# Performance work log

Measured on AMD Instinct MI355X. Metric: run time of the kernel, lower is better.

## Reference

```python
import jax, jax.numpy as jnp
import numpy as np

NUM_HEADS = 8

def _qkv(t, W, b, H):
    # t: [B, L, C] -> q, k, v each [B, H, L, D]
    B, L, C = t.shape
    D = C // H
    qkv = (t @ W + b).reshape(B, L, 3, H, D)
    qkv = jnp.moveaxis(qkv, 2, 0)           # [3, B, L, H, D]
    qkv = jnp.swapaxes(qkv, 2, 3)           # [3, B, H, L, D]
    return qkv[0], qkv[1], qkv[2]

def _attend(q, k, v, scale):
    # q,k,v: [B, H, L, D] -> [B, L, C]
    B, H, L, D = q.shape
    scores = jnp.einsum('bhqd,bhkd->bhqk', q, k) * scale
    attn = jax.nn.softmax(scores, axis=-1)
    out = jnp.einsum('bhqk,bhkd->bhqd', attn, v)
    return jnp.swapaxes(out, 1, 2).reshape(B, L, H * D)

def setup_inputs() -> dict:
    key = jax.random.key(0)
    ks = jax.random.split(key, 7)
    B, N, C = 8, 2048, 512
    s_in = 1.0 / np.sqrt(C)
    return {
        'x': jax.random.normal(ks[0], (B, N, C), dtype=jnp.float32),
        'W_rgb_qkv': jax.random.normal(ks[1], (C, 3 * C), dtype=jnp.float32) * s_in,
        'b_rgb_qkv': jax.random.normal(ks[2], (3 * C,), dtype=jnp.float32) * 0.02,
        'W_depth_qkv': jax.random.normal(ks[3], (C, 3 * C), dtype=jnp.float32) * s_in,
        'b_depth_qkv': jax.random.normal(ks[4], (3 * C,), dtype=jnp.float32) * 0.02,
        'W_proj': jax.random.normal(ks[5], (C, C), dtype=jnp.float32) * s_in,
        'b_proj': jax.random.normal(ks[6], (C,), dtype=jnp.float32) * 0.02,
    }

def reference(x, W_rgb_qkv, b_rgb_qkv, W_depth_qkv, b_depth_qkv, W_proj, b_proj):
    B, N, C = x.shape
    H = NUM_HEADS
    D = C // H
    scale = D ** -0.5
    L = N // 2
    rgb, depth = x[:, :L], x[:, L:]
    rq, rk, rv = _qkv(rgb, W_rgb_qkv, b_rgb_qkv, H)
    dq, dk, dv = _qkv(depth, W_depth_qkv, b_depth_qkv, H)
    # rgb queries attend to depth K/V (named depth_v in torch code)
    depth_out = _attend(rq, dk, dv, scale)
    # depth queries attend to rgb K/V (named rgb_v in torch code)
    rgb_out = _attend(dq, rk, rv, scale)
    out = jnp.concatenate([rgb_out, depth_out], axis=1)  # [B, N, C]
    return out @ W_proj + b_proj
```

## Files before the change

### kernel.cpp

```cpp
#include <hip/hip_runtime.h>
#include <hip/hip_bf16.h>

typedef __attribute__((ext_vector_type(8))) short s16x8;
typedef __attribute__((ext_vector_type(4))) float f32x4;

__device__ __forceinline__ ushort f2bf(float f) {
  union { float f; unsigned int u; } c; c.f = f;
  unsigned int u = c.u + 0x7fffu + ((c.u >> 16) & 1u);
  return (ushort)(u >> 16);
}

__device__ __forceinline__ unsigned int pack2(float lo, float hi) {
  __hip_bfloat162 b2 = __float22bfloat162_rn(make_float2(lo, hi));
  union { __hip_bfloat162 b; unsigned int u; } c; c.b = b2;
  return c.u;
}

__device__ __forceinline__ s16x8 ld16(const ushort* p) {
  union { uint4 u; s16x8 s; } c;
  c.u = *reinterpret_cast<const uint4*>(p);
  return c.s;
}

__device__ __forceinline__ f32x4 mfma16(s16x8 a, s16x8 b, f32x4 c) {
  return __builtin_amdgcn_mfma_f32_16x16x32_bf16(a, b, c, 0, 0, 0);
}

__device__ __forceinline__ float exp2fast(float x) { return __builtin_amdgcn_exp2f(x); }

__device__ __forceinline__ void gld_lds16(const void* g, void* l) {
  __builtin_amdgcn_global_load_lds(
      (const __attribute__((address_space(1))) void*)g,
      (__attribute__((address_space(3))) void*)l, 16, 0, 0);
}


__global__ __launch_bounds__(256) void k_prep(
    const float* __restrict__ x, ushort* __restrict__ xb,
    const float* __restrict__ Wr, ushort* __restrict__ WtR,
    const float* __restrict__ Wd, ushort* __restrict__ WtD,
    const float* __restrict__ Wp, ushort* __restrict__ WtP) {
  __shared__ float tile[32][33];
  int b = blockIdx.x, t = threadIdx.x;
  if (b < 8192) {
    int i = (b * 256 + t) * 4;
    float4 v = *reinterpret_cast<const float4*>(x + i);
    ushort4 o;
    o.x = f2bf(v.x); o.y = f2bf(v.y); o.z = f2bf(v.z); o.w = f2bf(v.w);
    *reinterpret_cast<ushort4*>(xb + i) = o;
    return;
  }
  b -= 8192;
  const float* src; ushort* dst; int N;
  if (b < 768)      { src = Wr; dst = WtR; N = 1536; }
  else if (b < 1536){ b -= 768;  src = Wd; dst = WtD; N = 1536; }
  else              { b -= 1536; src = Wp; dst = WtP; N = 512; }
  int nb = N >> 5;
  int n0 = (b % nb) * 32, k0 = (b / nb) * 32;
  int tx = t & 31, ty = t >> 5;
#pragma unroll
  for (int i = 0; i < 32; i += 8)
    tile[ty + i][tx] = src[(k0 + ty + i) * N + (n0 + tx)];
  __syncthreads();
#pragma unroll
  for (int i = 0; i < 32; i += 8)
    dst[(size_t)(n0 + ty + i) * 512 + (k0 + tx)] = f2bf(tile[tx][ty + i]);
}


__device__ __forceinline__ s16x8 lds_frag(const char* lds, int row, int c) {
  union { uint4 u; s16x8 s; } cv;
  cv.u = *reinterpret_cast<const uint4*>(lds + row * 128 + ((c ^ (row & 7)) * 16));
  return cv.s;
}

__device__ __forceinline__ s16x8 lds_frag32(const char* lds, int row, int c) {
  union { uint4 u; s16x8 s; } cv;
  cv.u = *reinterpret_cast<const uint4*>(lds + row * 64 + ((c ^ ((row >> 1) & 3)) * 16));
  return cv.s;
}

__device__ __forceinline__ void stage_lds(const ushort* __restrict__ src, int ld,
                                          char* ldsbase, int t) {
#pragma unroll
  for (int p = 0; p < 4; ++p) {
    int chunk = p * 256 + t;
    int r = chunk >> 3, cc = chunk & 7;
    gld_lds16(src + r * ld + ((cc ^ (r & 7)) * 8), ldsbase + (chunk & ~63) * 16);
  }
}


template <bool TRANS>
__global__ __launch_bounds__(256) void k_qkv(
    const ushort* __restrict__ xb, const ushort* __restrict__ WtR,
    const ushort* __restrict__ WtD, const float* __restrict__ bR,
    const float* __restrict__ bD, ushort* __restrict__ Qb,
    ushort* __restrict__ Kb, ushort* __restrict__ Vt) {
  __shared__ __align__(16) char lds[49152];
  int m0 = blockIdx.x * 128;
  int n0 = (TRANS ? 1024 : 0) + blockIdx.y * 128;
  int s = m0 >> 13, bb = (m0 >> 10) & 7, lbase = m0 & 1023;
  const ushort* A = xb + (size_t)(bb * 2048 + s * 1024 + lbase) * 512;
  const ushort* Wt = (s ? WtD : WtR) + (size_t)n0 * 512;
  const float* bias = s ? bD : bR;
  int t = threadIdx.x;
  int wid = t >> 6, ln = t & 15, g = (t & 63) >> 4;
  int wr = wid >> 1, wc = wid & 1;

  int r0 = t >> 2, c0 = t & 3;
  int r1 = (t + 256) >> 2, c1 = t & 3;
  int so0 = r0 * 512 + ((c0 ^ ((r0 >> 1) & 3)) * 8);
  int so1 = r1 * 512 + ((c1 ^ ((r1 >> 1) & 3)) * 8);
  int ldu = (t & ~63) * 16;

  const ushort* As = A;
  const ushort* Bs = Wt;
  char* b0 = lds;
  char* b1 = lds + 16384;
  char* b2 = lds + 32768;

  f32x4 acc[4][4] = {};

  gld_lds16(As + so0, b0 + ldu);
  gld_lds16(As + so1, b0 + 4096 + ldu);
  gld_lds16(Bs + so0, b0 + 8192 + ldu);
  gld_lds16(Bs + so1, b0 + 12288 + ldu);
  As += 32; Bs += 32;
  gld_lds16(As + so0, b1 + ldu);
  gld_lds16(As + so1, b1 + 4096 + ldu);
  gld_lds16(Bs + so0, b1 + 8192 + ldu);
  gld_lds16(Bs + so1, b1 + 12288 + ldu);
  As += 32; Bs += 32;
  asm volatile("s_waitcnt vmcnt(4)" ::: "memory");
  __builtin_amdgcn_sched_barrier(0);
  __builtin_amdgcn_s_barrier();
  __builtin_amdgcn_sched_barrier(0);

  for (int ks = 0; ks < 16; ++ks) {
    if (ks < 14) {
      gld_lds16(As + so0, b2 + ldu);
      gld_lds16(As + so1, b2 + 4096 + ldu);
      gld_lds16(Bs + so0, b2 + 8192 + ldu);
      gld_lds16(Bs + so1, b2 + 12288 + ldu);
      As += 32; Bs += 32;
    }
    s16x8 af[4], bf[4];
    __builtin_amdgcn_s_setprio(1);
#pragma unroll
    for (int mi = 0; mi < 4; ++mi) af[mi] = lds_frag32(b0, wr * 64 + mi * 16 + ln, g);
#pragma unroll
    for (int ni = 0; ni < 4; ++ni) bf[ni] = lds_frag32(b0 + 8192, wc * 64 + ni * 16 + ln, g);
#pragma unroll
    for (int mi = 0; mi < 4; ++mi)
#pragma unroll
      for (int ni = 0; ni < 4; ++ni)
        acc[mi][ni] = TRANS ? mfma16(bf[ni], af[mi], acc[mi][ni])
                            : mfma16(af[mi], bf[ni], acc[mi][ni]);
    __builtin_amdgcn_s_setprio(0);

    if (ks < 15) {
      if (ks < 14) {
        asm volatile("s_waitcnt vmcnt(4)" ::: "memory");
      } else {
        asm volatile("s_waitcnt vmcnt(0)" ::: "memory");
      }
      __builtin_amdgcn_sched_barrier(0);
      __builtin_amdgcn_s_barrier();
      __builtin_amdgcn_sched_barrier(0);
    }
    char* tmp = b0; b0 = b1; b1 = b2; b2 = tmp;
  }

  int hb_base = (s * 8 + bb) * 8;
  if (!TRANS) {
    bool isK = (n0 >> 9) != 0;
    ushort* dst = isK ? Kb : Qb;
    float sc = isK ? 1.0f : 0.18033688011112042f;
#pragma unroll
    for (int mi = 0; mi < 4; ++mi)
#pragma unroll
      for (int ni = 0; ni < 4; ++ni) {
        f32x4 v = acc[mi][ni];
        int col = n0 + wc * 64 + ni * 16 + ln;
        int h = (col >> 6) & 7, d = col & 63;
        float bv = bias[col];
        ushort* hp = dst + ((size_t)(hb_base + h) << 16);
        int lr = lbase + wr * 64 + mi * 16 + g * 4;
#pragma unroll
        for (int j = 0; j < 4; ++j) hp[(lr + j) * 64 + d] = f2bf((v[j] + bv) * sc);
      }
  } else {
    __syncthreads();
    ushort* et = (ushort*)lds;
#pragma unroll
    for (int mi = 0; mi < 4; ++mi) {
      int ll = wr * 64 + mi * 16 + ln;
      int lpl = (ll & ~63) | (ll & 0x23) | ((ll & 0x0C) << 1) | ((ll & 0x10) >> 2);
      int chunk = lpl >> 3, within = lpl & 7;
#pragma unroll
      for (int ni = 0; ni < 4; ++ni) {
        f32x4 v = acc[mi][ni];
        int crb = wc * 64 + ni * 16 + g * 4;
#pragma unroll
        for (int j = 0; j < 4; ++j) {
          int cr = crb + j;
          float bv = bias[n0 + cr];
          *(ushort*)((char*)et + cr * 256 + ((chunk ^ (cr & 15)) * 16) + within * 2)
              = f2bf(v[j] + bv);
        }
      }
    }
    __syncthreads();
#pragma unroll
    for (int pass = 0; pass < 8; ++pass) {
      int rrow = pass * 16 + (t >> 4);
      int c16 = t & 15;
      int col = n0 + rrow;
      int h = (col >> 6) & 7, d = col & 63;
      uint4 vv = *(const uint4*)((const char*)et + rrow * 256 + ((c16 ^ (rrow & 15)) * 16));
      *reinterpret_cast<uint4*>(Vt + ((size_t)(hb_base + h) << 16) + d * 1024 + lbase + c16 * 8)
          = vv;
    }
  }
}


__global__ __launch_bounds__(256) void k_attn(const ushort* __restrict__ Qb,
                                              const ushort* __restrict__ Kb,
                                              const ushort* __restrict__ Vt,
                                              ushort* __restrict__ AO) {
  __shared__ __align__(16) char lds[32768];
  int bid = blockIdx.x;
  int set = bid & 127, qb = bid >> 7;
  int pair = set & 1, h = (set >> 1) & 7, bb = set >> 4;
  int sQ = 1 - pair, sKV = pair;
  const ushort* Qp = Qb + ((size_t)((sQ * 8 + bb) * 8 + h) << 16);
  const ushort* Kp = Kb + ((size_t)((sKV * 8 + bb) * 8 + h) << 16);
  const ushort* Vp = Vt + ((size_t)((sKV * 8 + bb) * 8 + h) << 16);
  int t = threadIdx.x, w = t >> 6, ln = t & 15, g = (t & 63) >> 4;
  int q0 = qb * 128 + w * 32;
  s16x8 qf0a = ld16(Qp + (q0 + ln) * 64 + g * 8);
  s16x8 qf1a = ld16(Qp + (q0 + ln) * 64 + 32 + g * 8);
  s16x8 qf0b = ld16(Qp + (q0 + 16 + ln) * 64 + g * 8);
  s16x8 qf1b = ld16(Qp + (q0 + 16 + ln) * 64 + 32 + g * 8);

  int rA = t >> 3, ccA = t & 7;
  int rB = 32 + (t >> 3), ccB = t & 7;
  int kofA = rA * 64 + ((ccA ^ (rA & 7)) * 8);
  int kofB = rB * 64 + ((ccB ^ (rB & 7)) * 8);
  int vofA = rA * 1024 + ((ccA ^ (rA & 7)) * 8);
  int vofB = rB * 1024 + ((ccB ^ (rB & 7)) * 8);
  int ldst = (t & ~63) * 16;

  float ls_a = 0.f, ls_b = 0.f;
  f32x4 oca[4] = {}, ocb[4] = {};

  const ushort* kstage = Kp;
  const ushort* vstage = Vp;

  char* bc = lds;
  char* bn = lds + 16384;

  gld_lds16(kstage + kofA, bc + ldst);
  gld_lds16(kstage + kofB, bc + 4096 + ldst);
  gld_lds16(vstage + vofA, bc + 8192 + ldst);
  gld_lds16(vstage + vofB, bc + 12288 + ldst);
  kstage += 4096; vstage += 64;
  asm volatile("s_waitcnt vmcnt(0)" ::: "memory");
  __builtin_amdgcn_sched_barrier(0);
  __builtin_amdgcn_s_barrier();
  __builtin_amdgcn_sched_barrier(0);

  for (int it = 0; it < 16; ++it) {
    if (it < 15) {
      gld_lds16(kstage + kofA, bn + ldst);
      gld_lds16(kstage + kofB, bn + 4096 + ldst);
      gld_lds16(vstage + vofA, bn + 8192 + ldst);
      gld_lds16(vstage + vofB, bn + 12288 + ldst);
      kstage += 4096; vstage += 64;
    }

    f32x4 za[4], zb[4];
    __builtin_amdgcn_s_setprio(1);
#pragma unroll
    for (int s = 0; s < 4; ++s) {
      s16x8 k0 = lds_frag(bc, s * 16 + ln, g);
      s16x8 k1 = lds_frag(bc, s * 16 + ln, 4 + g);
      f32x4 z1 = {}; z1 = mfma16(k0, qf0a, z1); z1 = mfma16(k1, qf1a, z1); za[s] = z1;
      f32x4 z2 = {}; z2 = mfma16(k0, qf0b, z2); z2 = mfma16(k1, qf1b, z2); zb[s] = z2;
    }
    __builtin_amdgcn_s_setprio(0);

    unsigned int pwa[8], pwb[8];
#pragma unroll
    for (int s = 0; s < 4; ++s) {
      float p0 = exp2fast(za[s][0]), p1 = exp2fast(za[s][1]);
      float p2 = exp2fast(za[s][2]), p3 = exp2fast(za[s][3]);
      ls_a += (p0 + p1) + (p2 + p3);
      pwa[2 * s] = pack2(p0, p1); pwa[2 * s + 1] = pack2(p2, p3);
      float r0 = exp2fast(zb[s][0]), r1 = exp2fast(zb[s][1]);
      float r2 = exp2fast(zb[s][2]), r3 = exp2fast(zb[s][3]);
      ls_b += (r0 + r1) + (r2 + r3);
      pwb[2 * s] = pack2(r0, r1); pwb[2 * s + 1] = pack2(r2, r3);
    }
    union { uint4 u; s16x8 v; } c0, c1, c2, c3;
    c0.u = make_uint4(pwa[0], pwa[1], pwa[2], pwa[3]);
    c1.u = make_uint4(pwa[4], pwa[5], pwa[6], pwa[7]);
    c2.u = make_uint4(pwb[0], pwb[1], pwb[2], pwb[3]);
    c3.u = make_uint4(pwb[4], pwb[5], pwb[6], pwb[7]);
    s16x8 pf0a = c0.v, pf1a = c1.v, pf0b = c2.v, pf1b = c3.v;

    __builtin_amdgcn_s_setprio(1);
#pragma unroll
    for (int d = 0; d < 4; ++d) {
      s16x8 v0 = lds_frag(bc + 8192, d * 16 + ln, g);
      s16x8 v1 = lds_frag(bc + 8192, d * 16 + ln, 4 + g);
      oca[d] = mfma16(v0, pf0a, oca[d]);
      oca[d] = mfma16(v1, pf1a, oca[d]);
      ocb[d] = mfma16(v0, pf0b, ocb[d]);
      ocb[d] = mfma16(v1, pf1b, ocb[d]);
    }
    __builtin_amdgcn_s_setprio(0);

    if (it < 15) {
      asm volatile("s_waitcnt vmcnt(0)" ::: "memory");
      __builtin_amdgcn_sched_barrier(0);
      __builtin_amdgcn_s_barrier();
      __builtin_amdgcn_sched_barrier(0);
    }
    char* tmp = bc; bc = bn; bn = tmp;
  }

  ls_a += __shfl_xor(ls_a, 16, 64);
  ls_a += __shfl_xor(ls_a, 32, 64);
  ls_b += __shfl_xor(ls_b, 16, 64);
  ls_b += __shfl_xor(ls_b, 32, 64);
  float inva = 1.0f / ls_a, invb = 1.0f / ls_b;
  int orow = bb * 2048 + pair * 1024 + q0 + ln;
#pragma unroll
  for (int d = 0; d < 4; ++d) {
    uint2 st;
    st.x = pack2(oca[d][0] * inva, oca[d][1] * inva);
    st.y = pack2(oca[d][2] * inva, oca[d][3] * inva);
    *reinterpret_cast<uint2*>(AO + (size_t)orow * 512 + h * 64 + d * 16 + 4 * g) = st;
    uint2 st2;
    st2.x = pack2(ocb[d][0] * invb, ocb[d][1] * invb);
    st2.y = pack2(ocb[d][2] * invb, ocb[d][3] * invb);
    *reinterpret_cast<uint2*>(AO + (size_t)(orow + 16) * 512 + h * 64 + d * 16 + 4 * g) = st2;
  }
}


__global__ __launch_bounds__(256) void k_gemm_proj(const ushort* __restrict__ AO,
                                                   const ushort* __restrict__ WtP,
                                                   const float* __restrict__ bP,
                                                   float* __restrict__ Out) {
  __shared__ __align__(16) char lds[65536];
  int m0 = blockIdx.x * 128, n0 = blockIdx.y * 128;
  const ushort* A = AO + (size_t)m0 * 512;
  const ushort* Wt = WtP + (size_t)n0 * 512;
  int t = threadIdx.x;
  int wid = t >> 6, ln = t & 15, g = (t & 63) >> 4;
  int wr = wid >> 1, wc = wid & 1;
  f32x4 acc[4][4] = {};
  stage_lds(A, 512, lds, t);
  stage_lds(Wt, 512, lds + 16384, t);
  __syncthreads();
  for (int ks = 0; ks < 8; ++ks) {
    char* cbuf = lds + (ks & 1) * 32768;
    if (ks < 7) {
      char* nbuf = lds + ((ks + 1) & 1) * 32768;
      stage_lds(A + (ks + 1) * 64, 512, nbuf, t);
      stage_lds(Wt + (ks + 1) * 64, 512, nbuf + 16384, t);
    }
    char* ldsA = cbuf;
    char* ldsB = cbuf + 16384;
#pragma unroll
    for (int kk = 0; kk < 2; ++kk) {
      s16x8 af[4], bf[4];
#pragma unroll
      for (int mi = 0; mi < 4; ++mi) af[mi] = lds_frag(ldsA, wr * 64 + mi * 16 + ln, kk * 4 + g);
#pragma unroll
      for (int ni = 0; ni < 4; ++ni) bf[ni] = lds_frag(ldsB, wc * 64 + ni * 16 + ln, kk * 4 + g);
#pragma unroll
      for (int mi = 0; mi < 4; ++mi)
#pragma unroll
        for (int ni = 0; ni < 4; ++ni) acc[mi][ni] = mfma16(af[mi], bf[ni], acc[mi][ni]);
    }
    __syncthreads();
  }
#pragma unroll
  for (int mi = 0; mi < 4; ++mi)
#pragma unroll
    for (int ni = 0; ni < 4; ++ni) {
      f32x4 v = acc[mi][ni];
      int col = n0 + wc * 64 + ni * 16 + ln;
      float bv = bP[col];
      int r0 = m0 + wr * 64 + mi * 16 + g * 4;
#pragma unroll
      for (int j = 0; j < 4; ++j) Out[(size_t)(r0 + j) * 512 + col] = v[j] + bv;
    }
}


extern "C" void kernel_launch(void* const* d_in, const int* in_sizes, int n_in,
                              void* d_out, int out_size, void* d_ws, size_t ws_size,
                              hipStream_t stream) {
  const float* x      = (const float*)d_in[0];
  const float* W_rgb  = (const float*)d_in[1];
  const float* b_rgb  = (const float*)d_in[2];
  const float* W_dep  = (const float*)d_in[3];
  const float* b_dep  = (const float*)d_in[4];
  const float* W_proj = (const float*)d_in[5];
  const float* b_proj = (const float*)d_in[6];
  float* out = (float*)d_out;

  char* ws = (char*)d_ws;
  ushort* xb  = (ushort*)(ws + 0);
  ushort* WtR = (ushort*)(ws + 16777216);
  ushort* WtD = (ushort*)(ws + 18350080);
  ushort* WtP = (ushort*)(ws + 19922944);
  ushort* Qb  = (ushort*)(ws + 20447232);
  ushort* Kb  = (ushort*)(ws + 37224448);
  ushort* Vt  = (ushort*)(ws + 54001664);
  ushort* AO  = (ushort*)(ws + 70778880);

  k_prep<<<9984, 256, 0, stream>>>(x, xb, W_rgb, WtR, W_dep, WtD, W_proj, WtP);
  k_qkv<false><<<dim3(128, 8), 256, 0, stream>>>(xb, WtR, WtD, b_rgb, b_dep, Qb, Kb, Vt);
  k_qkv<true><<<dim3(128, 4), 256, 0, stream>>>(xb, WtR, WtD, b_rgb, b_dep, Qb, Kb, Vt);
  k_attn<<<1024, 256, 0, stream>>>(Qb, Kb, Vt, AO);
  k_gemm_proj<<<dim3(128, 4), 256, 0, stream>>>(AO, WtP, b_proj, out);
}
```

Before: 132.4 us.

## Split attention KV range across two wave groups and stage Q/K epilogue through LDS

The attention kernel now launches 512 threads per block. Two halves each process half of the key/value sequence with single-buffered LDS tiles, and their partial outputs and row sums are merged through shared memory at the end. The load-then-compute double buffering is replaced by load-after-barrier, which adds sync points per iteration. Separately, the Q/K projection epilogue now writes through a swizzled LDS tile so global stores become 16-byte rows instead of scattered 2-byte writes.

```diff
diff --git a/kernel.cpp b/kernel.cpp
--- a/kernel.cpp
+++ b/kernel.cpp
@@ -177,19 +177,34 @@
     bool isK = (n0 >> 9) != 0;
     ushort* dst = isK ? Kb : Qb;
     float sc = isK ? 1.0f : 0.18033688011112042f;
-#pragma unroll
-    for (int mi = 0; mi < 4; ++mi)
+    __syncthreads();
+    ushort* et = (ushort*)lds;
+#pragma unroll
+    for (int mi = 0; mi < 4; ++mi) {
 #pragma unroll
       for (int ni = 0; ni < 4; ++ni) {
         f32x4 v = acc[mi][ni];
-        int col = n0 + wc * 64 + ni * 16 + ln;
-        int h = (col >> 6) & 7, d = col & 63;
-        float bv = bias[col];
-        ushort* hp = dst + ((size_t)(hb_base + h) << 16);
-        int lr = lbase + wr * 64 + mi * 16 + g * 4;
-#pragma unroll
-        for (int j = 0; j < 4; ++j) hp[(lr + j) * 64 + d] = f2bf((v[j] + bv) * sc);
+        int cloc = wc * 64 + ni * 16 + ln;
+        float bv = bias[n0 + cloc];
+        int chunk = cloc >> 3, within = cloc & 7;
+#pragma unroll
+        for (int j = 0; j < 4; ++j) {
+          int lloc = wr * 64 + mi * 16 + g * 4 + j;
+          et[lloc * 128 + ((chunk ^ (lloc & 15)) * 8) + within] = f2bf((v[j] + bv) * sc);
+        }
       }
+    }
+    __syncthreads();
+#pragma unroll
+    for (int pass = 0; pass < 8; ++pass) {
+      int rrow = pass * 16 + (t >> 4);
+      int c16 = t & 15;
+      uint4 vv = *reinterpret_cast<const uint4*>(et + rrow * 128 + ((c16 ^ (rrow & 15)) * 8));
+      int col = n0 + c16 * 8;
+      int h = (col >> 6) & 7, d = col & 63;
+      *reinterpret_cast<uint4*>(dst + ((size_t)(hb_base + h) << 16) +
+                                (lbase + rrow) * 64 + d) = vv;
+    }
   } else {
     __syncthreads();
     ushort* et = (ushort*)lds;
@@ -226,11 +241,11 @@
 }
 
 
-__global__ __launch_bounds__(256) void k_attn(const ushort* __restrict__ Qb,
-                                              const ushort* __restrict__ Kb,
-                                              const ushort* __restrict__ Vt,
-                                              ushort* __restrict__ AO) {
-  __shared__ __align__(16) char lds[32768];
+__global__ __launch_bounds__(512, 6) void k_attn(const ushort* __restrict__ Qb,
+                                                 const ushort* __restrict__ Kb,
+                                                 const ushort* __restrict__ Vt,
+                                                 ushort* __restrict__ AO) {
+  __shared__ __align__(16) char lds[33280];
   int bid = blockIdx.x;
   int set = bid & 127, qb = bid >> 7;
   int pair = set & 1, h = (set >> 1) & 7, bb = set >> 4;
@@ -239,71 +254,59 @@
   const ushort* Kp = Kb + ((size_t)((sKV * 8 + bb) * 8 + h) << 16);
   const ushort* Vp = Vt + ((size_t)((sKV * 8 + bb) * 8 + h) << 16);
   int t = threadIdx.x, w = t >> 6, ln = t & 15, g = (t & 63) >> 4;
-  int q0 = qb * 128 + w * 32;
+  int kh = t >> 8;
+  int qg = w & 3;
+  int q0 = qb * 128 + qg * 32;
   s16x8 qf0a = ld16(Qp + (q0 + ln) * 64 + g * 8);
   s16x8 qf1a = ld16(Qp + (q0 + ln) * 64 + 32 + g * 8);
   s16x8 qf0b = ld16(Qp + (q0 + 16 + ln) * 64 + g * 8);
   s16x8 qf1b = ld16(Qp + (q0 + 16 + ln) * 64 + 32 + g * 8);
 
-  int rA = t >> 3, ccA = t & 7;
-  int rB = 32 + (t >> 3), ccB = t & 7;
-  int kofA = rA * 64 + ((ccA ^ (rA & 7)) * 8);
-  int kofB = rB * 64 + ((ccB ^ (rB & 7)) * 8);
-  int vofA = rA * 1024 + ((ccA ^ (rA & 7)) * 8);
-  int vofB = rB * 1024 + ((ccB ^ (rB & 7)) * 8);
-  int ldst = (t & ~63) * 16;
+  int c = t & 255;
+  int rA = c >> 3, cc = c & 7;
+  int rB = rA + 32;
+  int kofA = rA * 64 + ((cc ^ (rA & 7)) * 8);
+  int kofB = rB * 64 + ((cc ^ (rB & 7)) * 8);
+  int vofA = rA * 1024 + ((cc ^ (rA & 7)) * 8);
+  int vofB = rB * 1024 + ((cc ^ (rB & 7)) * 8);
+  char* hbase = lds + kh * 16384;
+  int wl = (w & 3) * 1024;
+
+  const ushort* ks = Kp + kh * 32768;
+  const ushort* vs = Vp + kh * 512;
 
   float ls_a = 0.f, ls_b = 0.f;
   f32x4 oca[4] = {}, ocb[4] = {};
 
-  const ushort* kstage = Kp;
-  const ushort* vstage = Vp;
-
-  char* bc = lds;
-  char* bn = lds + 16384;
-
-  gld_lds16(kstage + kofA, bc + ldst);
-  gld_lds16(kstage + kofB, bc + 4096 + ldst);
-  gld_lds16(vstage + vofA, bc + 8192 + ldst);
-  gld_lds16(vstage + vofB, bc + 12288 + ldst);
-  kstage += 4096; vstage += 64;
+  gld_lds16(ks + kofA, hbase + wl);
+  gld_lds16(ks + kofB, hbase + 4096 + wl);
+  gld_lds16(vs + vofA, hbase + 8192 + wl);
+  gld_lds16(vs + vofB, hbase + 12288 + wl);
+  ks += 4096; vs += 64;
   asm volatile("s_waitcnt vmcnt(0)" ::: "memory");
   __builtin_amdgcn_sched_barrier(0);
   __builtin_amdgcn_s_barrier();
   __builtin_amdgcn_sched_barrier(0);
 
-  for (int it = 0; it < 16; ++it) {
-    if (it < 15) {
-      gld_lds16(kstage + kofA, bn + ldst);
-      gld_lds16(kstage + kofB, bn + 4096 + ldst);
-      gld_lds16(vstage + vofA, bn + 8192 + ldst);
-      gld_lds16(vstage + vofB, bn + 12288 + ldst);
-      kstage += 4096; vstage += 64;
-    }
-
-    f32x4 za[4], zb[4];
+  for (int it = 0; it < 8; ++it) {
+    unsigned int pwa[8], pwb[8];
     __builtin_amdgcn_s_setprio(1);
 #pragma unroll
     for (int s = 0; s < 4; ++s) {
-      s16x8 k0 = lds_frag(bc, s * 16 + ln, g);
-      s16x8 k1 = lds_frag(bc, s * 16 + ln, 4 + g);
-      f32x4 z1 = {}; z1 = mfma16(k0, qf0a, z1); z1 = mfma16(k1, qf1a, z1); za[s] = z1;
-      f32x4 z2 = {}; z2 = mfma16(k0, qf0b, z2); z2 = mfma16(k1, qf1b, z2); zb[s] = z2;
-    }
-    __builtin_amdgcn_s_setprio(0);
-
-    unsigned int pwa[8], pwb[8];
-#pragma unroll
-    for (int s = 0; s < 4; ++s) {
-      float p0 = exp2fast(za[s][0]), p1 = exp2fast(za[s][1]);
-      float p2 = exp2fast(za[s][2]), p3 = exp2fast(za[s][3]);
+      s16x8 k0 = lds_frag(hbase, s * 16 + ln, g);
+      s16x8 k1 = lds_frag(hbase, s * 16 + ln, 4 + g);
+      f32x4 z1 = {}; z1 = mfma16(k0, qf0a, z1); z1 = mfma16(k1, qf1a, z1);
+      f32x4 z2 = {}; z2 = mfma16(k0, qf0b, z2); z2 = mfma16(k1, qf1b, z2);
+      float p0 = exp2fast(z1[0]), p1 = exp2fast(z1[1]);
+      float p2 = exp2fast(z1[2]), p3 = exp2fast(z1[3]);
       ls_a += (p0 + p1) + (p2 + p3);
       pwa[2 * s] = pack2(p0, p1); pwa[2 * s + 1] = pack2(p2, p3);
-      float r0 = exp2fast(zb[s][0]), r1 = exp2fast(zb[s][1]);
-      float r2 = exp2fast(zb[s][2]), r3 = exp2fast(zb[s][3]);
+      float r0 = exp2fast(z2[0]), r1 = exp2fast(z2[1]);
+      float r2 = exp2fast(z2[2]), r3 = exp2fast(z2[3]);
       ls_b += (r0 + r1) + (r2 + r3);
       pwb[2 * s] = pack2(r0, r1); pwb[2 * s + 1] = pack2(r2, r3);
     }
+    __builtin_amdgcn_s_setprio(0);
     union { uint4 u; s16x8 v; } c0, c1, c2, c3;
     c0.u = make_uint4(pwa[0], pwa[1], pwa[2], pwa[3]);
     c1.u = make_uint4(pwa[4], pwa[5], pwa[6], pwa[7]);
@@ -314,8 +317,8 @@
     __builtin_amdgcn_s_setprio(1);
 #pragma unroll
     for (int d = 0; d < 4; ++d) {
-      s16x8 v0 = lds_frag(bc + 8192, d * 16 + ln, g);
-      s16x8 v1 = lds_frag(bc + 8192, d * 16 + ln, 4 + g);
+      s16x8 v0 = lds_frag(hbase + 8192, d * 16 + ln, g);
+      s16x8 v1 = lds_frag(hbase + 8192, d * 16 + ln, 4 + g);
       oca[d] = mfma16(v0, pf0a, oca[d]);
       oca[d] = mfma16(v1, pf1a, oca[d]);
       ocb[d] = mfma16(v0, pf0b, ocb[d]);
@@ -323,31 +326,67 @@
     }
     __builtin_amdgcn_s_setprio(0);
 
-    if (it < 15) {
+    __builtin_amdgcn_sched_barrier(0);
+    __builtin_amdgcn_s_barrier();
+    __builtin_amdgcn_sched_barrier(0);
+    if (it < 7) {
+      gld_lds16(ks + kofA, hbase + wl);
+      gld_lds16(ks + kofB, hbase + 4096 + wl);
+      gld_lds16(vs + vofA, hbase + 8192 + wl);
+      gld_lds16(vs + vofB, hbase + 12288 + wl);
+      ks += 4096; vs += 64;
       asm volatile("s_waitcnt vmcnt(0)" ::: "memory");
       __builtin_amdgcn_sched_barrier(0);
       __builtin_amdgcn_s_barrier();
       __builtin_amdgcn_sched_barrier(0);
     }
-    char* tmp = bc; bc = bn; bn = tmp;
   }
 
   ls_a += __shfl_xor(ls_a, 16, 64);
   ls_a += __shfl_xor(ls_a, 32, 64);
   ls_b += __shfl_xor(ls_b, 16, 64);
   ls_b += __shfl_xor(ls_b, 32, 64);
-  float inva = 1.0f / ls_a, invb = 1.0f / ls_b;
-  int orow = bb * 2048 + pair * 1024 + q0 + ln;
-#pragma unroll
-  for (int d = 0; d < 4; ++d) {
-    uint2 st;
-    st.x = pack2(oca[d][0] * inva, oca[d][1] * inva);
-    st.y = pack2(oca[d][2] * inva, oca[d][3] * inva);
-    *reinterpret_cast<uint2*>(AO + (size_t)orow * 512 + h * 64 + d * 16 + 4 * g) = st;
-    uint2 st2;
-    st2.x = pack2(ocb[d][0] * invb, ocb[d][1] * invb);
-    st2.y = pack2(ocb[d][2] * invb, ocb[d][3] * invb);
-    *reinterpret_cast<uint2*>(AO + (size_t)(orow + 16) * 512 + h * 64 + d * 16 + 4 * g) = st2;
+
+  float* obuf = (float*)lds;
+  float* lsbuf = (float*)(lds + 32768);
+  if (kh == 1) {
+    int rowa = (qg * 2) * 16 + ln;
+    int rowb = rowa + 16;
+#pragma unroll
+    for (int d = 0; d < 4; ++d) {
+      int chka = ((d * 4 + g) ^ ln) * 4;
+      *reinterpret_cast<float4*>(&obuf[rowa * 64 + chka]) =
+          make_float4(oca[d][0], oca[d][1], oca[d][2], oca[d][3]);
+      *reinterpret_cast<float4*>(&obuf[rowb * 64 + chka]) =
+          make_float4(ocb[d][0], ocb[d][1], ocb[d][2], ocb[d][3]);
+    }
+    if (g == 0) {
+      lsbuf[rowa] = ls_a;
+      lsbuf[rowb] = ls_b;
+    }
+  }
+  __syncthreads();
+  if (kh == 0) {
+    int rowa = (qg * 2) * 16 + ln;
+    int rowb = rowa + 16;
+    ls_a += lsbuf[rowa];
+    ls_b += lsbuf[rowb];
+    float inva = 1.0f / ls_a, invb = 1.0f / ls_b;
+    int orow = bb * 2048 + pair * 1024 + q0 + ln;
+#pragma unroll
+    for (int d = 0; d < 4; ++d) {
+      int chka = ((d * 4 + g) ^ ln) * 4;
+      float4 va = *reinterpret_cast<const float4*>(&obuf[rowa * 64 + chka]);
+      float4 vb = *reinterpret_cast<const float4*>(&obuf[rowb * 64 + chka]);
+      uint2 st;
+      st.x = pack2((oca[d][0] + va.x) * inva, (oca[d][1] + va.y) * inva);
+      st.y = pack2((oca[d][2] + va.z) * inva, (oca[d][3] + va.w) * inva);
+      *reinterpret_cast<uint2*>(AO + (size_t)orow * 512 + h * 64 + d * 16 + 4 * g) = st;
+      uint2 st2;
+      st2.x = pack2((ocb[d][0] + vb.x) * invb, (ocb[d][1] + vb.y) * invb);
+      st2.y = pack2((ocb[d][2] + vb.z) * invb, (ocb[d][3] + vb.w) * invb);
+      *reinterpret_cast<uint2*>(AO + (size_t)(orow + 16) * 512 + h * 64 + d * 16 + 4 * g) = st2;
+    }
   }
 }
 
@@ -429,6 +468,6 @@
   k_prep<<<9984, 256, 0, stream>>>(x, xb, W_rgb, WtR, W_dep, WtD, W_proj, WtP);
   k_qkv<false><<<dim3(128, 8), 256, 0, stream>>>(xb, WtR, WtD, b_rgb, b_dep, Qb, Kb, Vt);
   k_qkv<true><<<dim3(128, 4), 256, 0, stream>>>(xb, WtR, WtD, b_rgb, b_dep, Qb, Kb, Vt);
-  k_attn<<<1024, 256, 0, stream>>>(Qb, Kb, Vt, AO);
+  k_attn<<<1024, 512, 0, stream>>>(Qb, Kb, Vt, AO);
   k_gemm_proj<<<dim3(128, 4), 256, 0, stream>>>(AO, WtP, b_proj, out);
 }
```

Result: slower. 394.0 us (+197.5%).
